# Optimization experiments

Measured on AMD Instinct MI355X. Metric: run time of the kernel, lower is better.

## Reference

```python
import jax, jax.numpy as jnp
import numpy as np

D_IN = 256
D_PROJ = 256
N = 8192


def setup_inputs() -> dict:
    key = jax.random.key(0)
    ks = jax.random.split(key, 7)
    s = 1.0 / np.sqrt(D_IN)
    return {
        "x": jax.random.normal(ks[0], (N, D_IN), dtype=jnp.float32),
        "Wq": jax.random.uniform(ks[1], (D_IN, D_PROJ), jnp.float32, -s, s),
        "bq": jax.random.uniform(ks[2], (D_PROJ,), jnp.float32, -s, s),
        "Wk": jax.random.uniform(ks[3], (D_IN, D_PROJ), jnp.float32, -s, s),
        "bk": jax.random.uniform(ks[4], (D_PROJ,), jnp.float32, -s, s),
        "Wv": jax.random.uniform(ks[5], (D_IN, D_PROJ), jnp.float32, -s, s),
        "bv": jax.random.uniform(ks[6], (D_PROJ,), jnp.float32, -s, s),
    }


def reference(x, Wq, bq, Wk, bk, Wv, bv):
    # x: [N, D_IN]
    q = x @ Wq + bq          # [N, D]
    k = x @ Wk + bk          # [N, D]
    v = x @ Wv + bv          # [N, D]
    scale = 1.0 / jnp.sqrt(jnp.asarray(D_PROJ, dtype=x.dtype))
    scores = (q @ k.T) * scale              # [N, N]
    weights = jax.nn.softmax(scores, axis=-1)
    return weights @ v                       # [N, D]
```

## Files before the change

### kernel.cpp

```cpp
#include <hip/hip_runtime.h>


typedef float f32x16 __attribute__((ext_vector_type(16)));
typedef short s16x8  __attribute__((ext_vector_type(8)));

typedef __attribute__((address_space(1))) void g1v;
typedef __attribute__((address_space(3))) void l3v;

__device__ __forceinline__ short f2bf(float f) {
  unsigned u = __float_as_uint(f);
  u += 0x7fffu + ((u >> 16) & 1u);
  return (short)(u >> 16);
}
__device__ __forceinline__ float bf2f(short s) {
  return __uint_as_float(((unsigned)(unsigned short)s) << 16);
}
__device__ __forceinline__ void gl16(const void* g, void* l) {
  __builtin_amdgcn_global_load_lds((g1v*)g, (l3v*)l, 16, 0, 0);
}
__device__ __forceinline__ f32x16 mfma32(s16x8 a, s16x8 b, f32x16 c) {
  return __builtin_amdgcn_mfma_f32_32x32x16_bf16(a, b, c, 0, 0, 0);
}

__global__ void prep_k(const float* __restrict__ Wq, const float* __restrict__ Wk,
                       const float* __restrict__ Wv, short* __restrict__ Wt) {
  __shared__ short tl[32][33];
  const int b = blockIdx.x;
  const int m = b >> 6, tile = b & 63;
  const int r0 = (tile >> 3) * 32, c0 = (tile & 7) * 32;
  const float* W = (m == 0) ? Wq : (m == 1) ? Wk : Wv;
  short* dst = Wt + m * 65536;
  const int tx = threadIdx.x & 31, ty = threadIdx.x >> 5;
#pragma unroll
  for (int j = 0; j < 4; ++j) tl[ty * 4 + j][tx] = f2bf(W[(r0 + ty * 4 + j) * 256 + c0 + tx]);
  __syncthreads();
#pragma unroll
  for (int j = 0; j < 4; ++j) {
    const int c = ty * 4 + j;
    dst[(c0 + c) * 256 + r0 + tx] = tl[tx][c];
  }
}

__global__ __launch_bounds__(256, 2) void proj_k(
    const float* __restrict__ x, const short* __restrict__ Wt,
    const float* __restrict__ bq, const float* __restrict__ bk,
    const float* __restrict__ bv,
    short* __restrict__ Qb, short* __restrict__ Kb, short* __restrict__ Vb) {
  __shared__ short xl[8192];
  const int tid = threadIdx.x;
  const int m = blockIdx.x >> 8, rb = blockIdx.x & 255;
  {
    const int r = tid >> 3, seg = tid & 7;
    const int sw = (r & 15) << 3;
    const float* xp = x + (size_t)(rb * 32 + r) * 256 + seg * 32;
#pragma unroll
    for (int i = 0; i < 4; ++i) {
      float4 f0 = *(const float4*)(xp + i * 8);
      float4 f1 = *(const float4*)(xp + i * 8 + 4);
      s16x8 v;
      v[0] = f2bf(f0.x); v[1] = f2bf(f0.y); v[2] = f2bf(f0.z); v[3] = f2bf(f0.w);
      v[4] = f2bf(f1.x); v[5] = f2bf(f1.y); v[6] = f2bf(f1.z); v[7] = f2bf(f1.w);
      const int e = seg * 32 + i * 8;
      *(s16x8*)&xl[r * 256 + (e ^ sw)] = v;
    }
  }
  __syncthreads();
  const int l = tid & 63, w = tid >> 6;
  const int r31 = l & 31, g = l >> 5;
  const int ksw = (r31 & 15) << 3;
  const short* xlp = &xl[0] + r31 * 256;
  const float* bp = (m == 0) ? bq : (m == 1) ? bk : bv;
  short* outp = (m == 0) ? Qb : (m == 1) ? Kb : Vb;
#pragma unroll
  for (int jj = 0; jj < 2; ++jj) {
    const int ct = w * 2 + jj;
    const short* wp = Wt + m * 65536 + (ct * 32 + r31) * 256 + g * 8;
    f32x16 ta, tb;
#pragma unroll
    for (int j = 0; j < 16; ++j) { ta[j] = 0.f; tb[j] = 0.f; }
#pragma unroll
    for (int c = 0; c < 8; ++c) {
      s16x8 xa = *(const s16x8*)(xlp + ((c * 16 + g * 8) ^ ksw));
      s16x8 wf = *(const s16x8*)(wp + c * 16);
      ta = mfma32(xa, wf, ta);
    }
#pragma unroll
    for (int c = 8; c < 16; ++c) {
      s16x8 xa = *(const s16x8*)(xlp + ((c * 16 + g * 8) ^ ksw));
      s16x8 wf = *(const s16x8*)(wp + c * 16);
      tb = mfma32(xa, wf, tb);
    }
    const float bias = bp[ct * 32 + r31];
#pragma unroll
    for (int i = 0; i < 16; ++i) {
      const int row = (i & 3) + 8 * (i >> 2) + 4 * g;
      outp[(size_t)(rb * 32 + row) * 256 + ct * 32 + r31] = f2bf(ta[i] + tb[i] + bias);
    }
  }
}

__global__ __launch_bounds__(256) void prep_vt(const short* __restrict__ Vb,
                                               short* __restrict__ Vt) {
  const int kvt = blockIdx.x, d = threadIdx.x;
  const short* src = Vb + (size_t)kvt * 32 * 256 + d;
  short* dst = Vt + (size_t)d * 8192 + kvt * 32;
#pragma unroll
  for (int i = 0; i < 4; ++i) {
    s16x8 v;
#pragma unroll
    for (int j = 0; j < 8; ++j) {
      const int p = i * 8 + j;
      const int sig = (p & 0x13) | ((p & 4) << 1) | ((p & 8) >> 1);
      v[j] = src[(size_t)sig * 256];
    }
    *(s16x8*)(dst + i * 8) = v;
  }
}

__device__ __forceinline__ void stage_kt(const short* Kg, int kvbase,
                                         short* kbuf, int tid) {
#pragma unroll
  for (int rnd = 0; rnd < 4; ++rnd) {
    const int r = rnd * 8 + (tid >> 5);
    const int e = (tid & 31) * 8;
    gl16(Kg + (size_t)(kvbase + r) * 256 + (e ^ ((r & 15) << 3)),
         kbuf + (rnd * 256 + tid) * 8);
  }
}
__device__ __forceinline__ void stage_vt(const short* Vt, int kvbase,
                                         short* vbuf, int tid) {
#pragma unroll
  for (int rnd = 0; rnd < 4; ++rnd) {
    const int slot = rnd * 256 + tid;
    const int row = slot >> 2, sp4 = slot & 3;
    gl16(Vt + (size_t)row * 8192 + kvbase + ((sp4 ^ ((row >> 2) & 3)) << 3),
         vbuf + slot * 8);
  }
}

__global__ __launch_bounds__(256, 2) void attn_k(
    const short* __restrict__ Qb, const short* __restrict__ Kb,
    const short* __restrict__ Vt, short* __restrict__ Opb,
    float* __restrict__ rsg) {
  __shared__ short Kl[2][8192];
  __shared__ short Vl[2][8192];
  const int tid = threadIdx.x;
  const int w = tid >> 6, l = tid & 63;
  const int r31 = l & 31, g = l >> 5;
  const int sp = blockIdx.x & 7, qb = blockIdx.x >> 3;
  const int kv0 = sp << 10;

  s16x8 qf[16];
  {
    const short* qp = Qb + (size_t)(qb * 128 + w * 32 + r31) * 256 + g * 8;
#pragma unroll
    for (int c = 0; c < 16; ++c) qf[c] = *(const s16x8*)(qp + c * 16);
  }

  f32x16 o[8];
#pragma unroll
  for (int i = 0; i < 8; ++i) {
#pragma unroll
    for (int j = 0; j < 16; ++j) o[i][j] = 0.f;
  }
  float rsum = 0.f;

  stage_kt(Kb, kv0, &Kl[0][0], tid);
  stage_vt(Vt, kv0, &Vl[0][0], tid);
  __syncthreads();

  const int ksw = (r31 & 15) << 3;
  const int f4 = (r31 >> 2) & 3;
  const int x0 = (g ^ f4) << 3;
  const int x1 = ((2 | g) ^ f4) << 3;

#pragma unroll 1
  for (int t = 0; t < 32; ++t) {
    const int cur = t & 1, nxt = cur ^ 1;
    if (t < 31) {
      stage_kt(Kb, kv0 + (t + 1) * 32, &Kl[nxt][0], tid);
      stage_vt(Vt, kv0 + (t + 1) * 32, &Vl[nxt][0], tid);
    }
    const short* klp = &Kl[cur][0] + r31 * 256;
    f32x16 ta, tb;
#pragma unroll
    for (int j = 0; j < 16; ++j) { ta[j] = 0.f; tb[j] = 0.f; }
    __builtin_amdgcn_s_setprio(1);
#pragma unroll
    for (int c = 0; c < 8; ++c) {
      s16x8 kf = *(const s16x8*)(klp + ((c * 16 + g * 8) ^ ksw));
      ta = mfma32(kf, qf[c], ta);
    }
#pragma unroll
    for (int c = 8; c < 16; ++c) {
      s16x8 kf = *(const s16x8*)(klp + ((c * 16 + g * 8) ^ ksw));
      tb = mfma32(kf, qf[c], tb);
    }
    __builtin_amdgcn_s_setprio(0);
    s16x8 pa0, pa1;
#pragma unroll
    for (int i = 0; i < 8; ++i) {
      float p0 = __expf((ta[i] + tb[i]) * 0.0625f);
      float p1 = __expf((ta[i + 8] + tb[i + 8]) * 0.0625f);
      rsum += p0 + p1;
      pa0[i] = f2bf(p0);
      pa1[i] = f2bf(p1);
    }
    const short* vlp = &Vl[cur][0] + r31 * 32;
    __builtin_amdgcn_s_setprio(1);
#pragma unroll
    for (int dt = 0; dt < 8; ++dt) {
      s16x8 b0 = *(const s16x8*)(vlp + dt * 1024 + x0);
      s16x8 b1 = *(const s16x8*)(vlp + dt * 1024 + x1);
      o[dt] = mfma32(pa0, b0, o[dt]);
      o[dt] = mfma32(pa1, b1, o[dt]);
    }
    __builtin_amdgcn_s_setprio(0);
    __syncthreads();
  }

  rsum += __shfl_xor(rsum, 32);
  if (l < 32) rsg[sp * 8192 + qb * 128 + w * 32 + l] = rsum;
  short* op = Opb + (size_t)sp * 2097152 + (size_t)(qb * 128 + w * 32) * 256;
#pragma unroll
  for (int dt = 0; dt < 8; ++dt) {
#pragma unroll
    for (int i = 0; i < 16; ++i) {
      const int row = (i & 3) + 8 * (i >> 2) + 4 * g;
      op[row * 256 + dt * 32 + r31] = f2bf(o[dt][i]);
    }
  }
}

__global__ __launch_bounds__(256, 8) void comb_k(const short* __restrict__ Opb,
                                                 const float* __restrict__ rsg,
                                                 float* __restrict__ out) {
  const int i8 = (blockIdx.x * 256 + threadIdx.x) * 8;
  const int n = i8 >> 8;
  float acc[8];
#pragma unroll
  for (int j = 0; j < 8; ++j) acc[j] = 0.f;
  float rt = 0.f;
#pragma unroll
  for (int sp = 0; sp < 8; ++sp) {
    const s16x8 v = *(const s16x8*)(Opb + (size_t)sp * 2097152 + i8);
#pragma unroll
    for (int j = 0; j < 8; ++j) acc[j] += bf2f(v[j]);
    rt += rsg[sp * 8192 + n];
  }
  const float inv = 1.f / rt;
  float4 r0, r1;
  r0.x = acc[0] * inv; r0.y = acc[1] * inv; r0.z = acc[2] * inv; r0.w = acc[3] * inv;
  r1.x = acc[4] * inv; r1.y = acc[5] * inv; r1.z = acc[6] * inv; r1.w = acc[7] * inv;
  *(float4*)(out + i8) = r0;
  *(float4*)(out + i8 + 4) = r1;
}

extern "C" void kernel_launch(void* const* d_in, const int* in_sizes, int n_in,
                              void* d_out, int out_size, void* d_ws,
                              size_t ws_size, hipStream_t stream) {
  const float* x  = (const float*)d_in[0];
  const float* Wq = (const float*)d_in[1];
  const float* bq = (const float*)d_in[2];
  const float* Wk = (const float*)d_in[3];
  const float* bk = (const float*)d_in[4];
  const float* Wv = (const float*)d_in[5];
  const float* bv = (const float*)d_in[6];
  float* out = (float*)d_out;

  char* ws = (char*)d_ws;
  short* Wt  = (short*)ws;
  float* rsg = (float*)(ws + 393216u);
  short* Qb  = (short*)(ws + 655360u);
  short* Kb  = Qb + 2097152;
  short* Vt  = Kb + 2097152;
  short* Vb  = Vt + 2097152;
  short* Opb = Vb;

  hipLaunchKernelGGL(prep_k, dim3(192), dim3(256), 0, stream, Wq, Wk, Wv, Wt);
  hipLaunchKernelGGL(proj_k, dim3(768), dim3(256), 0, stream, x, Wt, bq, bk, bv,
                     Qb, Kb, Vb);
  hipLaunchKernelGGL(prep_vt, dim3(256), dim3(256), 0, stream, Vb, Vt);
  hipLaunchKernelGGL(attn_k, dim3(512), dim3(256), 0, stream, Qb, Kb, Vt, Opb,
                     rsg);
  hipLaunchKernelGGL(comb_k, dim3(1024), dim3(256), 0, stream, Opb, rsg, out);
}
```

Before: 200.4 us.

## Fuse V transpose into projection and prefetch two KV tiles ahead

The V projection blocks now write their tile to shared memory and emit the transposed Vt layout directly, which removes the separate prep_vt launch and the intermediate Vb round trip through global memory. The attention loop changes from a one-ahead double buffer to a depth-two prefetch using explicit vmcnt waits and raw barriers, so loads for tile t+2 are issued right after tile t finishes. The aim is to hide global-to-LDS latency better and cut one kernel launch. In exchange it relies on hand-written waitcnt accounting, where a wrong count could race.

```diff
diff --git a/kernel.cpp b/kernel.cpp
--- a/kernel.cpp
+++ b/kernel.cpp
@@ -21,6 +21,9 @@
 __device__ __forceinline__ f32x16 mfma32(s16x8 a, s16x8 b, f32x16 c) {
   return __builtin_amdgcn_mfma_f32_32x32x16_bf16(a, b, c, 0, 0, 0);
 }
+__device__ __forceinline__ void wait_vm8()  { asm volatile("s_waitcnt vmcnt(8)" ::: "memory"); }
+__device__ __forceinline__ void wait_vm0()  { asm volatile("s_waitcnt vmcnt(0)" ::: "memory"); }
+__device__ __forceinline__ void wait_lgkm0(){ asm volatile("s_waitcnt lgkmcnt(0)" ::: "memory"); }
 
 __global__ void prep_k(const float* __restrict__ Wq, const float* __restrict__ Wk,
                        const float* __restrict__ Wv, short* __restrict__ Wt) {
@@ -45,7 +48,7 @@
     const float* __restrict__ x, const short* __restrict__ Wt,
     const float* __restrict__ bq, const float* __restrict__ bk,
     const float* __restrict__ bv,
-    short* __restrict__ Qb, short* __restrict__ Kb, short* __restrict__ Vb) {
+    short* __restrict__ Qb, short* __restrict__ Kb, short* __restrict__ Vt) {
   __shared__ short xl[8192];
   const int tid = threadIdx.x;
   const int m = blockIdx.x >> 8, rb = blockIdx.x & 255;
@@ -70,7 +73,7 @@
   const int ksw = (r31 & 15) << 3;
   const short* xlp = &xl[0] + r31 * 256;
   const float* bp = (m == 0) ? bq : (m == 1) ? bk : bv;
-  short* outp = (m == 0) ? Qb : (m == 1) ? Kb : Vb;
+  float res[2][16];
 #pragma unroll
   for (int jj = 0; jj < 2; ++jj) {
     const int ct = w * 2 + jj;
@@ -92,28 +95,44 @@
     }
     const float bias = bp[ct * 32 + r31];
 #pragma unroll
-    for (int i = 0; i < 16; ++i) {
-      const int row = (i & 3) + 8 * (i >> 2) + 4 * g;
-      outp[(size_t)(rb * 32 + row) * 256 + ct * 32 + r31] = f2bf(ta[i] + tb[i] + bias);
-    }
-  }
-}
-
-__global__ __launch_bounds__(256) void prep_vt(const short* __restrict__ Vb,
-                                               short* __restrict__ Vt) {
-  const int kvt = blockIdx.x, d = threadIdx.x;
-  const short* src = Vb + (size_t)kvt * 32 * 256 + d;
-  short* dst = Vt + (size_t)d * 8192 + kvt * 32;
-#pragma unroll
-  for (int i = 0; i < 4; ++i) {
-    s16x8 v;
-#pragma unroll
-    for (int j = 0; j < 8; ++j) {
-      const int p = i * 8 + j;
-      const int sig = (p & 0x13) | ((p & 4) << 1) | ((p & 8) >> 1);
-      v[j] = src[(size_t)sig * 256];
-    }
-    *(s16x8*)(dst + i * 8) = v;
+    for (int i = 0; i < 16; ++i) res[jj][i] = ta[i] + tb[i] + bias;
+  }
+  if (m < 2) {
+    short* outp = (m == 0) ? Qb : Kb;
+#pragma unroll
+    for (int jj = 0; jj < 2; ++jj) {
+      const int ct = w * 2 + jj;
+#pragma unroll
+      for (int i = 0; i < 16; ++i) {
+        const int row = (i & 3) + 8 * (i >> 2) + 4 * g;
+        outp[(size_t)(rb * 32 + row) * 256 + ct * 32 + r31] = f2bf(res[jj][i]);
+      }
+    }
+  } else {
+    __syncthreads();
+#pragma unroll
+    for (int jj = 0; jj < 2; ++jj) {
+      const int ct = w * 2 + jj;
+#pragma unroll
+      for (int i = 0; i < 16; ++i) {
+        const int row = (i & 3) + 8 * (i >> 2) + 4 * g;
+        xl[row * 256 + ct * 32 + r31] = f2bf(res[jj][i]);
+      }
+    }
+    __syncthreads();
+    const int d = tid;
+    short* dst = Vt + (size_t)d * 8192 + rb * 32;
+#pragma unroll
+    for (int i = 0; i < 4; ++i) {
+      s16x8 v;
+#pragma unroll
+      for (int j = 0; j < 8; ++j) {
+        const int p = i * 8 + j;
+        const int sig = (p & 0x13) | ((p & 4) << 1) | ((p & 8) >> 1);
+        v[j] = xl[sig * 256 + d];
+      }
+      *(s16x8*)(dst + i * 8) = v;
+    }
   }
 }
 
@@ -167,7 +186,8 @@
 
   stage_kt(Kb, kv0, &Kl[0][0], tid);
   stage_vt(Vt, kv0, &Vl[0][0], tid);
-  __syncthreads();
+  stage_kt(Kb, kv0 + 32, &Kl[1][0], tid);
+  stage_vt(Vt, kv0 + 32, &Vl[1][0], tid);
 
   const int ksw = (r31 & 15) << 3;
   const int f4 = (r31 >> 2) & 3;
@@ -176,11 +196,10 @@
 
 #pragma unroll 1
   for (int t = 0; t < 32; ++t) {
-    const int cur = t & 1, nxt = cur ^ 1;
-    if (t < 31) {
-      stage_kt(Kb, kv0 + (t + 1) * 32, &Kl[nxt][0], tid);
-      stage_vt(Vt, kv0 + (t + 1) * 32, &Vl[nxt][0], tid);
-    }
+    const int cur = t & 1;
+    if (t < 31) wait_vm8(); else wait_vm0();
+    __builtin_amdgcn_s_barrier();
+    __builtin_amdgcn_sched_barrier(0);
     const short* klp = &Kl[cur][0] + r31 * 256;
     f32x16 ta, tb;
 #pragma unroll
@@ -216,7 +235,13 @@
       o[dt] = mfma32(pa1, b1, o[dt]);
     }
     __builtin_amdgcn_s_setprio(0);
-    __syncthreads();
+    wait_lgkm0();
+    __builtin_amdgcn_s_barrier();
+    __builtin_amdgcn_sched_barrier(0);
+    if (t < 30) {
+      stage_kt(Kb, kv0 + (t + 2) * 32, &Kl[cur][0], tid);
+      stage_vt(Vt, kv0 + (t + 2) * 32, &Vl[cur][0], tid);
+    }
   }
 
   rsum += __shfl_xor(rsum, 32);
@@ -274,13 +299,11 @@
   short* Qb  = (short*)(ws + 655360u);
   short* Kb  = Qb + 2097152;
   short* Vt  = Kb + 2097152;
-  short* Vb  = Vt + 2097152;
-  short* Opb = Vb;
+  short* Opb = Vt + 2097152;
 
   hipLaunchKernelGGL(prep_k, dim3(192), dim3(256), 0, stream, Wq, Wk, Wv, Wt);
   hipLaunchKernelGGL(proj_k, dim3(768), dim3(256), 0, stream, x, Wt, bq, bk, bv,
-                     Qb, Kb, Vb);
-  hipLaunchKernelGGL(prep_vt, dim3(256), dim3(256), 0, stream, Vb, Vt);
+                     Qb, Kb, Vt);
   hipLaunchKernelGGL(attn_k, dim3(512), dim3(256), 0, stream, Qb, Kb, Vt, Opb,
                      rsg);
   hipLaunchKernelGGL(comb_k, dim3(1024), dim3(256), 0, stream, Opb, rsg, out);
```

Result: faster. 186.3 us (-7.0%).
